# Kernel optimization log

Hardware: AMD Instinct MI355X
Metric: run time of the kernel (lower is better)

The kernel has to match this reference:

```python
import jax, jax.numpy as jnp
import numpy as np

B, N, D = 4, 512, 256  # batch, num_diseases, feature_dim == hidden_dim
H = 256                # hidden_dim
EPS = 1e-5

def _layernorm(x, g, b):
    m = jnp.mean(x, axis=-1, keepdims=True)
    v = jnp.mean((x - m) ** 2, axis=-1, keepdims=True)
    return (x - m) * jax.lax.rsqrt(v + EPS) * g + b

def setup_inputs() -> dict:
    key = jax.random.key(0)
    ks = jax.random.split(key, 16)
    s = 0.02
    return {
        "x": jax.random.normal(ks[0], (B, N, D), jnp.float32),
        "area_matrix": jax.random.uniform(ks[1], (B, N), jnp.float32),
        "co_occurrence": jax.random.uniform(ks[2], (N, N), jnp.float32),
        "Wq": jax.random.normal(ks[3], (H, D), jnp.float32) * s,
        "bq": jnp.zeros((H,), jnp.float32),
        "Wk": jax.random.normal(ks[4], (H, D), jnp.float32) * s,
        "bk": jnp.zeros((H,), jnp.float32),
        "Wv": jax.random.normal(ks[5], (H, D), jnp.float32) * s,
        "bv": jnp.zeros((H,), jnp.float32),
        "We1": jax.random.normal(ks[6], (H, 2), jnp.float32) * 0.5,
        "be1": jnp.zeros((H,), jnp.float32),
        "We2": jax.random.normal(ks[7], (1, H), jnp.float32) * s,
        "be2": jnp.zeros((1,), jnp.float32),
        "Wo": jax.random.normal(ks[8], (H, H), jnp.float32) * s,
        "bo": jnp.zeros((H,), jnp.float32),
        "g_ot": jnp.ones((H,), jnp.float32),
        "b_ot": jnp.zeros((H,), jnp.float32),
        "g1": jnp.ones((H,), jnp.float32),
        "b1": jnp.zeros((H,), jnp.float32),
        "g2": jnp.ones((H,), jnp.float32),
        "b2": jnp.zeros((H,), jnp.float32),
    }

def reference(x, area_matrix, co_occurrence, Wq, bq, Wk, bk, Wv, bv,
              We1, be1, We2, be2, Wo, bo, g_ot, b_ot, g1, b1, g2, b2):
    # projections: (B, N, H)
    q = jnp.einsum('bnd,hd->bnh', x, Wq) + bq
    k = jnp.einsum('bnd,hd->bnh', x, Wk) + bk
    v = jnp.einsum('bnd,hd->bnh', x, Wv) + bv
    attn_scores = jnp.einsum('bih,bjh->bij', q, k) / jnp.sqrt(jnp.float32(H))
    # edge inputs: (B, N, N, 2) = stack(broadcast area along last N, broadcast co-occ along batch)
    area = jnp.broadcast_to(area_matrix[:, :, None], (B, N, N))
    co = jnp.broadcast_to(co_occurrence[None], (B, N, N))
    edge_inputs = jnp.stack([area, co], axis=-1)
    h = jax.nn.relu(jnp.einsum('bije,he->bijh', edge_inputs, We1) + be1)
    edge_weights = jax.nn.sigmoid(jnp.einsum('bijh,oh->bijo', h, We2) + be2)[..., 0]
    attn_probs = jax.nn.softmax(attn_scores * edge_weights, axis=-1)  # dropout = identity (eval)
    out = jnp.einsum('bij,bjh->bih', attn_probs, v)
    out = _layernorm(out, g1, b1)
    out = jax.nn.relu(_layernorm(jnp.einsum('bnh,oh->bno', out, Wo) + bo, g_ot, b_ot))
    out = _layernorm(out + x, g2, b2)
    return out
```

## Files before the change

kernel.cpp:

```cpp
#include <hip/hip_runtime.h>

typedef unsigned short u16;
typedef unsigned int u32;

#define NB 4
#define NN 512
#define ND 256
#define NH 256
#define TI 4

typedef __attribute__((ext_vector_type(8))) short short8;
typedef __attribute__((ext_vector_type(4))) float f32x4;

__device__ __forceinline__ u16 bfq(float f) {
    u32 t; __builtin_memcpy(&t, &f, 4);
    u32 r = (t + 0x7FFFu + ((t >> 16) & 1u)) >> 16;
    return (u16)r;
}

__device__ __forceinline__ float waveReduceSum(float v) {
#pragma unroll
    for (int o = 32; o > 0; o >>= 1) v += __shfl_down(v, o);
    return v;
}

__device__ __forceinline__ void blockReduce8(float4& va, float4& vb, float4* red) {
#pragma unroll
    for (int o = 32; o > 0; o >>= 1) {
        va.x += __shfl_down(va.x, o); va.y += __shfl_down(va.y, o);
        va.z += __shfl_down(va.z, o); va.w += __shfl_down(va.w, o);
        vb.x += __shfl_down(vb.x, o); vb.y += __shfl_down(vb.y, o);
        vb.z += __shfl_down(vb.z, o); vb.w += __shfl_down(vb.w, o);
    }
    int wid = threadIdx.x >> 6;
    __syncthreads();
    if ((threadIdx.x & 63) == 0) { red[2 * wid] = va; red[2 * wid + 1] = vb; }
    __syncthreads();
    float4 ra = red[0], rb = red[1];
#pragma unroll
    for (int w = 1; w < 8; ++w) {
        float4 ua = red[2 * w], ub = red[2 * w + 1];
        ra.x += ua.x; ra.y += ua.y; ra.z += ua.z; ra.w += ua.w;
        rb.x += ub.x; rb.y += ub.y; rb.z += ub.z; rb.w += ub.w;
    }
    va = ra; vb = rb;
}

__global__ __launch_bounds__(256) void prep_kernel(
    const float* __restrict__ x, const float* __restrict__ Wq,
    const float* __restrict__ Wk, const float* __restrict__ Wv,
    const float* __restrict__ Wo,
    u16* __restrict__ xb, u16* __restrict__ wb)
{
    const int idx4 = (blockIdx.x * 256 + threadIdx.x) * 4;
    const float* src;
    u16* dst;
    int off;
    if (idx4 < 524288) { src = x; dst = xb; off = idx4; }
    else {
        int u = idx4 - 524288;
        int which = u >> 16; off = u & 65535;
        src = (which == 0) ? Wq : (which == 1) ? Wk : (which == 2) ? Wv : Wo;
        dst = wb + which * 65536;
    }
    float4 f = *(const float4*)(src + off);
    u32 lo = (u32)bfq(f.x) | ((u32)bfq(f.y) << 16);
    u32 hi = (u32)bfq(f.z) | ((u32)bfq(f.w) << 16);
    *(uint2*)(dst + off) = make_uint2(lo, hi);
}

__global__ __launch_bounds__(256) void qkv_mfma(
    const u16* __restrict__ xb, const u16* __restrict__ wb,
    const float* __restrict__ bq, const float* __restrict__ bk, const float* __restrict__ bv,
    u16* __restrict__ qb, u16* __restrict__ kb, u16* __restrict__ vt)
{
    const int lane = threadIdx.x & 63, wave = threadIdx.x >> 6;
    const int r0 = blockIdx.x * 64 + wave * 16;
    const int out0 = blockIdx.y * 16;
    const int which = blockIdx.y >> 4;
    const float* bia = (which == 0) ? bq : (which == 1) ? bk : bv;

    const int m = lane & 15, koff = (lane >> 4) * 8;
    const u16* Ap = xb + (size_t)(r0 + m) * 256 + koff;
    const u16* Bp = wb + which * 65536 + (size_t)((out0 & 255) + m) * 256 + koff;

    f32x4 acc = {0.f, 0.f, 0.f, 0.f};
#pragma unroll
    for (int ks = 0; ks < 8; ++ks) {
        short8 a  = *(const short8*)(Ap + ks * 32);
        short8 bb = *(const short8*)(Bp + ks * 32);
        acc = __builtin_amdgcn_mfma_f32_16x16x32_bf16(a, bb, acc, 0, 0, 0);
    }

    const int oc = (out0 + m) & 255;
    const float bias = bia[oc];
    const int rbase = r0 + (lane >> 4) * 4;
#pragma unroll
    for (int reg = 0; reg < 4; ++reg) {
        int R = rbase + reg;
        u16 val = bfq(acc[reg] + bias);
        if (which == 0)      qb[(size_t)R * 256 + oc] = val;
        else if (which == 1) kb[(size_t)R * 256 + oc] = val;
        else                 vt[((size_t)(R >> 9) * 256 + oc) * 512 + (R & 511)] = val;
    }
}

#define PSTR 520
#define YSTR 264
__global__ __launch_bounds__(512) void fused_kernel(
    const float* __restrict__ x, const float* __restrict__ area, const float* __restrict__ co,
    const float* __restrict__ We1, const float* __restrict__ be1,
    const float* __restrict__ We2, const float* __restrict__ be2,
    const u16* __restrict__ wob, const float* __restrict__ bo,
    const float* __restrict__ g_ot, const float* __restrict__ b_ot,
    const float* __restrict__ g1, const float* __restrict__ b1,
    const float* __restrict__ g2, const float* __restrict__ b2,
    const u16* __restrict__ qb, const u16* __restrict__ kb,
    const u16* __restrict__ vt, float* __restrict__ out)
{
    const int tid = threadIdx.x;
    const int b = blockIdx.x >> 7;
    const int i0 = (blockIdx.x & 127) << 2;
    const int lane = tid & 63, w = tid >> 6;

    __shared__ float histS[1024], histB[1024];
    __shared__ float pvbuf[1024];
    __shared__ u16 srow16[16 * PSTR];
    __shared__ u16 y16[16 * YSTR];
    __shared__ float4 red8b[16];
    __shared__ float sBaseS[4], sBaseB[4], redA[8], redB[8];

    const float be2f = be2[0];

    histS[tid] = 0.f; histS[tid + 512] = 0.f;
    histB[tid] = 0.f; histB[tid + 512] = 0.f;
    {
        u32* s32 = (u32*)srow16;
        for (int i = tid; i < 4160; i += 512) s32[i] = 0u;
        u32* y32 = (u32*)y16;
        for (int i = tid; i < 2112; i += 512) y32[i] = 0u;
    }
    __syncthreads();

    {
        const int s = tid >> 7, h0 = tid & 127;
        const float a = area[b * NN + i0 + s];
        float baS = 0.f, baB = 0.f;
#pragma unroll
        for (int k = 0; k < 2; ++k) {
            const int h = h0 + 128 * k;
            const float w10 = We1[2 * h], w11 = We1[2 * h + 1];
            const float w2v = We2[h], be1v = be1[h];
            const float al = fmaf(a, w10, be1v);
            const float sl = w11 * w2v, bb = al * w2v;
            if (w11 == 0.f) {
                if (al > 0.f) baB += bb;
            } else {
                float tt = -al / w11;
                if (w11 > 0.f) {
                    if (tt <= 0.f)      { baS += sl; baB += bb; }
                    else if (tt < 1.f) {
                        int u = (int)(tt * 256.f); u = u > 255 ? 255 : u;
                        atomicAdd(&histS[s * 256 + u], sl);
                        atomicAdd(&histB[s * 256 + u], bb);
                    }
                } else {
                    if (tt >= 1.f)      { baS += sl; baB += bb; }
                    else if (tt > 0.f) {
                        baS += sl; baB += bb;
                        int u = (int)(tt * 256.f); u = u > 255 ? 255 : u;
                        atomicAdd(&histS[s * 256 + u], -sl);
                        atomicAdd(&histB[s * 256 + u], -bb);
                    }
                }
            }
        }
        float rS = waveReduceSum(baS), rB = waveReduceSum(baB);
        if (lane == 0) { redA[w] = rS; redB[w] = rB; }
    }

    f32x4 sacc[4];
    {
        const int m = lane & 15, koff = (lane >> 4) * 8;
        const u16* Ap = qb + (size_t)(b * 512 + i0 + m) * 256 + koff;
        short8 afr[8];
#pragma unroll
        for (int ks = 0; ks < 8; ++ks) afr[ks] = *(const short8*)(Ap + ks * 32);
#pragma unroll
        for (int t = 0; t < 4; ++t) {
            const int j0 = (w * 4 + t) * 16;
            const u16* Bp = kb + (size_t)(b * 512 + j0 + m) * 256 + koff;
            f32x4 acc = {0.f, 0.f, 0.f, 0.f};
#pragma unroll
            for (int ks = 0; ks < 8; ++ks) {
                short8 bb = *(const short8*)(Bp + ks * 32);
                acc = __builtin_amdgcn_mfma_f32_16x16x32_bf16(afr[ks], bb, acc, 0, 0, 0);
            }
            sacc[t] = acc;
        }
    }
    __syncthreads();
    if (tid < 4) {
        sBaseS[tid] = redA[2 * tid] + redA[2 * tid + 1];
        sBaseB[tid] = redB[2 * tid] + redB[2 * tid + 1];
    }

    {
        const int s = w & 3;
        float* hp = (w < 4) ? histS : histB;
        float b0 = hp[s * 256 + 4 * lane + 0];
        float b1 = hp[s * 256 + 4 * lane + 1];
        float b2 = hp[s * 256 + 4 * lane + 2];
        float b3 = hp[s * 256 + 4 * lane + 3];
        float p0 = b0, p1 = p0 + b1, p2 = p1 + b2, p3 = p2 + b3;
        float incl = p3;
#pragma unroll
        for (int off = 1; off < 64; off <<= 1) {
            float t = __shfl_up(incl, off);
            if (lane >= off) incl += t;
        }
        float excl = incl - p3;
        hp[s * 256 + 4 * lane + 0] = p0 + excl;
        hp[s * 256 + 4 * lane + 1] = p1 + excl;
        hp[s * 256 + 4 * lane + 2] = p2 + excl;
        hp[s * 256 + 4 * lane + 3] = p3 + excl;
    }
    __syncthreads();

    if (lane < 16) {
#pragma unroll
        for (int t = 0; t < 4; ++t) {
            const int j = (w * 4 + t) * 16 + lane;
#pragma unroll
            for (int reg = 0; reg < 4; ++reg) {
                float c = co[(size_t)(i0 + reg) * NN + j];
                int u = (int)(c * 256.f); u = u > 255 ? 255 : u;
                float Sg = sBaseS[reg] + histS[reg * 256 + u];
                float Bg = sBaseB[reg] + histB[reg * 256 + u];
                float e = fmaf(c, Sg, Bg) + be2f;
                float ew = 1.f / (1.f + __expf(-e));
                srow16[reg * PSTR + j] = bfq(__expf(sacc[t][reg] * 0.0625f * ew));
            }
        }
    }
    __syncthreads();

    {
        const int m = lane & 15, koff = (lane >> 4) * 8;
        const int t0 = 2 * w, t1 = 2 * w + 1;
        const u16* B0p = vt + ((size_t)(b * 256 + t0 * 16 + m)) * 512 + koff;
        const u16* B1p = vt + ((size_t)(b * 256 + t1 * 16 + m)) * 512 + koff;
        const u16* Arow = srow16 + m * PSTR + koff;
        f32x4 acc0 = {0.f, 0.f, 0.f, 0.f}, acc1 = {0.f, 0.f, 0.f, 0.f};
#pragma unroll
        for (int ks = 0; ks < 16; ++ks) {
            short8 a  = *(const short8*)(Arow + ks * 32);
            short8 b0 = *(const short8*)(B0p + ks * 32);
            short8 b1 = *(const short8*)(B1p + ks * 32);
            acc0 = __builtin_amdgcn_mfma_f32_16x16x32_bf16(a, b0, acc0, 0, 0, 0);
            acc1 = __builtin_amdgcn_mfma_f32_16x16x32_bf16(a, b1, acc1, 0, 0, 0);
        }
        __syncthreads();
        if (lane < 16) {
#pragma unroll
            for (int reg = 0; reg < 4; ++reg) {
                pvbuf[reg * 256 + t0 * 16 + lane] = acc0[reg];
                pvbuf[reg * 256 + t1 * 16 + lane] = acc1[reg];
            }
        }
        __syncthreads();
    }

    const int hP = tid & 255, half = tid >> 8;
    float4 sa, sb;
    float accv[TI];
#pragma unroll
    for (int ti = 0; ti < TI; ++ti) {
        accv[ti] = (half == 0) ? pvbuf[ti * 256 + hP] : 0.f;
        ((float*)&sa)[ti] = accv[ti];
        ((float*)&sb)[ti] = accv[ti] * accv[ti];
    }
    blockReduce8(sa, sb, red8b);
    if (half == 0) {
        const float g1v = g1[hP], b1v = b1[hP];
#pragma unroll
        for (int ti = 0; ti < TI; ++ti) {
            float mean = ((const float*)&sa)[ti] * (1.f / 256.f);
            float var = fmaxf(((const float*)&sb)[ti] * (1.f / 256.f) - mean * mean, 0.f);
            y16[ti * YSTR + hP] = bfq((accv[ti] - mean) * rsqrtf(var + 1e-5f) * g1v + b1v);
        }
    }
    __syncthreads();

    {
        const int m = lane & 15, koff = (lane >> 4) * 8;
        const int t0 = 2 * w, t1 = 2 * w + 1;
        const u16* B0p = wob + (size_t)(t0 * 16 + m) * 256 + koff;
        const u16* B1p = wob + (size_t)(t1 * 16 + m) * 256 + koff;
        const u16* Arow = y16 + m * YSTR + koff;
        f32x4 acc0 = {0.f, 0.f, 0.f, 0.f}, acc1 = {0.f, 0.f, 0.f, 0.f};
#pragma unroll
        for (int ks = 0; ks < 8; ++ks) {
            short8 a  = *(const short8*)(Arow + ks * 32);
            short8 b0 = *(const short8*)(B0p + ks * 32);
            short8 b1 = *(const short8*)(B1p + ks * 32);
            acc0 = __builtin_amdgcn_mfma_f32_16x16x32_bf16(a, b0, acc0, 0, 0, 0);
            acc1 = __builtin_amdgcn_mfma_f32_16x16x32_bf16(a, b1, acc1, 0, 0, 0);
        }
        __syncthreads();
        if (lane < 16) {
#pragma unroll
            for (int reg = 0; reg < 4; ++reg) {
                pvbuf[reg * 256 + t0 * 16 + lane] = acc0[reg];
                pvbuf[reg * 256 + t1 * 16 + lane] = acc1[reg];
            }
        }
        __syncthreads();
    }

    float acc2[TI];
    {
        const float bov = (half == 0) ? bo[hP] : 0.f;
#pragma unroll
        for (int ti = 0; ti < TI; ++ti) {
            acc2[ti] = (half == 0) ? pvbuf[ti * 256 + hP] + bov : 0.f;
            ((float*)&sa)[ti] = acc2[ti];
            ((float*)&sb)[ti] = acc2[ti] * acc2[ti];
        }
    }
    blockReduce8(sa, sb, red8b);
    float z[TI];
    const float gotv = (half == 0) ? g_ot[hP] : 0.f;
    const float botv = (half == 0) ? b_ot[hP] : 0.f;
#pragma unroll
    for (int ti = 0; ti < TI; ++ti) {
        float mean = ((const float*)&sa)[ti] * (1.f / 256.f);
        float var = fmaxf(((const float*)&sb)[ti] * (1.f / 256.f) - mean * mean, 0.f);
        z[ti] = fmaxf((acc2[ti] - mean) * rsqrtf(var + 1e-5f) * gotv + botv, 0.f);
    }

    float tt[TI];
#pragma unroll
    for (int ti = 0; ti < TI; ++ti) {
        tt[ti] = (half == 0) ? z[ti] + x[(size_t)(b * NN + i0 + ti) * ND + hP] : 0.f;
        ((float*)&sa)[ti] = tt[ti]; ((float*)&sb)[ti] = tt[ti] * tt[ti];
    }
    blockReduce8(sa, sb, red8b);
    if (half == 0) {
        const float g2v = g2[hP], b2v = b2[hP];
#pragma unroll
        for (int ti = 0; ti < TI; ++ti) {
            float mean = ((const float*)&sa)[ti] * (1.f / 256.f);
            float var = fmaxf(((const float*)&sb)[ti] * (1.f / 256.f) - mean * mean, 0.f);
            float o = (tt[ti] - mean) * rsqrtf(var + 1e-5f) * g2v + b2v;
            out[(size_t)(b * NN + i0 + ti) * NH + hP] = o;
        }
    }
}

extern "C" void kernel_launch(void* const* d_in, const int* in_sizes, int n_in,
                              void* d_out, int out_size, void* d_ws, size_t ws_size,
                              hipStream_t stream) {
    const float* x    = (const float*)d_in[0];
    const float* area = (const float*)d_in[1];
    const float* co   = (const float*)d_in[2];
    const float* Wq   = (const float*)d_in[3];
    const float* bq   = (const float*)d_in[4];
    const float* Wk   = (const float*)d_in[5];
    const float* bk   = (const float*)d_in[6];
    const float* Wv   = (const float*)d_in[7];
    const float* bv   = (const float*)d_in[8];
    const float* We1  = (const float*)d_in[9];
    const float* be1  = (const float*)d_in[10];
    const float* We2  = (const float*)d_in[11];
    const float* be2  = (const float*)d_in[12];
    const float* Wo   = (const float*)d_in[13];
    const float* bo   = (const float*)d_in[14];
    const float* g_ot = (const float*)d_in[15];
    const float* b_ot = (const float*)d_in[16];
    const float* g1   = (const float*)d_in[17];
    const float* b1   = (const float*)d_in[18];
    const float* g2   = (const float*)d_in[19];
    const float* b2   = (const float*)d_in[20];

    u16*  xb  = (u16*)d_ws;
    u16*  wb  = xb + (size_t)2048 * 256;
    u16*  qb  = wb + (size_t)4 * 65536;
    u16*  kb  = qb + (size_t)2048 * 256;
    u16*  vt  = kb + (size_t)2048 * 256;

    prep_kernel<<<768, 256, 0, stream>>>(x, Wq, Wk, Wv, Wo, xb, wb);
    qkv_mfma<<<dim3(32, 48), 256, 0, stream>>>(xb, wb, bq, bk, bv, qb, kb, vt);
    fused_kernel<<<NB * NN / TI, 512, 0, stream>>>(x, area, co, We1, be1, We2, be2,
                                                   wb + 3 * 65536, bo,
                                                   g_ot, b_ot, g1, b1, g2, b2,
                                                   qb, kb, vt, (float*)d_out);
}
```

Measured before the change: 162.0 us.

## Prefetch global loads early, double-buffer K fragments, spread edge-weight work across lanes

Loads of the Q and K fragments, the co-occurrence values, x, and all per-channel parameters are moved to the top of the kernel so their latency overlaps the histogram phase. The QK^T loop now double-buffers K fragments in two halves so loads overlap the MFMAs. The edge-weight and exp step uses all 64 lanes via shuffles instead of only 16. Two barriers before the pvbuf writes are removed, and launch bounds now request 4 blocks. Register pressure rises from holding the prefetched values, and the occupancy hint may cause spills.

```diff
diff --git a/kernel.cpp b/kernel.cpp
--- a/kernel.cpp
+++ b/kernel.cpp
@@ -107,7 +107,7 @@
 
 #define PSTR 520
 #define YSTR 264
-__global__ __launch_bounds__(512) void fused_kernel(
+__global__ __launch_bounds__(512, 4) void fused_kernel(
     const float* __restrict__ x, const float* __restrict__ area, const float* __restrict__ co,
     const float* __restrict__ We1, const float* __restrict__ be1,
     const float* __restrict__ We2, const float* __restrict__ be2,
@@ -122,6 +122,8 @@
     const int b = blockIdx.x >> 7;
     const int i0 = (blockIdx.x & 127) << 2;
     const int lane = tid & 63, w = tid >> 6;
+    const int g = lane >> 4, c = lane & 15;
+    const int hP = tid & 255, half = tid >> 8;
 
     __shared__ float histS[1024], histB[1024];
     __shared__ float pvbuf[1024];
@@ -130,6 +132,32 @@
     __shared__ float4 red8b[16];
     __shared__ float sBaseS[4], sBaseB[4], redA[8], redB[8];
 
+    const int m = lane & 15, koff = (lane >> 4) * 8;
+    const u16* Ap    = qb + (size_t)(b * 512 + i0 + m) * 256 + koff;
+    const u16* Kbase = kb + (size_t)(b * 512 + m) * 256 + koff;
+
+    short8 afr[8];
+#pragma unroll
+    for (int ks = 0; ks < 8; ++ks) afr[ks] = *(const short8*)(Ap + ks * 32);
+    short8 k0[4], k1[4];
+#pragma unroll
+    for (int ks = 0; ks < 4; ++ks)
+        k0[ks] = *(const short8*)(Kbase + (size_t)(w * 4) * 16 * 256 + ks * 32);
+
+    float cov[4];
+#pragma unroll
+    for (int t = 0; t < 4; ++t)
+        cov[t] = co[(size_t)(i0 + g) * NN + (w * 4 + t) * 16 + c];
+
+    float xv[TI];
+#pragma unroll
+    for (int ti = 0; ti < TI; ++ti)
+        xv[ti] = x[(size_t)(b * NN + i0 + ti) * ND + hP];
+
+    const float bov  = bo[hP];
+    const float g1v  = g1[hP],  b1v  = b1[hP];
+    const float gotv = g_ot[hP], botv = b_ot[hP];
+    const float g2v  = g2[hP],  b2v  = b2[hP];
     const float be2f = be2[0];
 
     histS[tid] = 0.f; histS[tid + 512] = 0.f;
@@ -181,21 +209,23 @@
 
     f32x4 sacc[4];
     {
-        const int m = lane & 15, koff = (lane >> 4) * 8;
-        const u16* Ap = qb + (size_t)(b * 512 + i0 + m) * 256 + koff;
-        short8 afr[8];
-#pragma unroll
-        for (int ks = 0; ks < 8; ++ks) afr[ks] = *(const short8*)(Ap + ks * 32);
 #pragma unroll
         for (int t = 0; t < 4; ++t) {
-            const int j0 = (w * 4 + t) * 16;
-            const u16* Bp = kb + (size_t)(b * 512 + j0 + m) * 256 + koff;
+            const u16* Bp = Kbase + (size_t)(w * 4 + t) * 16 * 256;
+#pragma unroll
+            for (int ks = 0; ks < 4; ++ks) k1[ks] = *(const short8*)(Bp + (ks + 4) * 32);
             f32x4 acc = {0.f, 0.f, 0.f, 0.f};
 #pragma unroll
-            for (int ks = 0; ks < 8; ++ks) {
-                short8 bb = *(const short8*)(Bp + ks * 32);
-                acc = __builtin_amdgcn_mfma_f32_16x16x32_bf16(afr[ks], bb, acc, 0, 0, 0);
+            for (int ks = 0; ks < 4; ++ks)
+                acc = __builtin_amdgcn_mfma_f32_16x16x32_bf16(afr[ks], k0[ks], acc, 0, 0, 0);
+            if (t < 3) {
+                const u16* Bn = Kbase + (size_t)(w * 4 + t + 1) * 16 * 256;
+#pragma unroll
+                for (int ks = 0; ks < 4; ++ks) k0[ks] = *(const short8*)(Bn + ks * 32);
             }
+#pragma unroll
+            for (int ks = 0; ks < 4; ++ks)
+                acc = __builtin_amdgcn_mfma_f32_16x16x32_bf16(afr[ks + 4], k1[ks], acc, 0, 0, 0);
             sacc[t] = acc;
         }
     }
@@ -227,26 +257,27 @@
     }
     __syncthreads();
 
-    if (lane < 16) {
+    {
 #pragma unroll
         for (int t = 0; t < 4; ++t) {
-            const int j = (w * 4 + t) * 16 + lane;
-#pragma unroll
-            for (int reg = 0; reg < 4; ++reg) {
-                float c = co[(size_t)(i0 + reg) * NN + j];
-                int u = (int)(c * 256.f); u = u > 255 ? 255 : u;
-                float Sg = sBaseS[reg] + histS[reg * 256 + u];
-                float Bg = sBaseB[reg] + histB[reg * 256 + u];
-                float e = fmaf(c, Sg, Bg) + be2f;
-                float ew = 1.f / (1.f + __expf(-e));
-                srow16[reg * PSTR + j] = bfq(__expf(sacc[t][reg] * 0.0625f * ew));
-            }
-        }
-    }
-    __syncthreads();
-
-    {
-        const int m = lane & 15, koff = (lane >> 4) * 8;
+            const int j = (w * 4 + t) * 16 + c;
+            float s0 = __shfl(sacc[t][0], c);
+            float s1 = __shfl(sacc[t][1], c);
+            float s2 = __shfl(sacc[t][2], c);
+            float s3 = __shfl(sacc[t][3], c);
+            float sv = (g == 0) ? s0 : (g == 1) ? s1 : (g == 2) ? s2 : s3;
+            float cc = cov[t];
+            int u = (int)(cc * 256.f); u = u > 255 ? 255 : u;
+            float Sg = sBaseS[g] + histS[g * 256 + u];
+            float Bg = sBaseB[g] + histB[g * 256 + u];
+            float e = fmaf(cc, Sg, Bg) + be2f;
+            float ew = 1.f / (1.f + __expf(-e));
+            srow16[g * PSTR + j] = bfq(__expf(sv * 0.0625f * ew));
+        }
+    }
+    __syncthreads();
+
+    {
         const int t0 = 2 * w, t1 = 2 * w + 1;
         const u16* B0p = vt + ((size_t)(b * 256 + t0 * 16 + m)) * 512 + koff;
         const u16* B1p = vt + ((size_t)(b * 256 + t1 * 16 + m)) * 512 + koff;
@@ -260,7 +291,6 @@
             acc0 = __builtin_amdgcn_mfma_f32_16x16x32_bf16(a, b0, acc0, 0, 0, 0);
             acc1 = __builtin_amdgcn_mfma_f32_16x16x32_bf16(a, b1, acc1, 0, 0, 0);
         }
-        __syncthreads();
         if (lane < 16) {
 #pragma unroll
             for (int reg = 0; reg < 4; ++reg) {
@@ -271,7 +301,6 @@
         __syncthreads();
     }
 
-    const int hP = tid & 255, half = tid >> 8;
     float4 sa, sb;
     float accv[TI];
 #pragma unroll
@@ -282,7 +311,6 @@
     }
     blockReduce8(sa, sb, red8b);
     if (half == 0) {
-        const float g1v = g1[hP], b1v = b1[hP];
 #pragma unroll
         for (int ti = 0; ti < TI; ++ti) {
             float mean = ((const float*)&sa)[ti] * (1.f / 256.f);
@@ -293,7 +321,6 @@
     __syncthreads();
 
     {
-        const int m = lane & 15, koff = (lane >> 4) * 8;
         const int t0 = 2 * w, t1 = 2 * w + 1;
         const u16* B0p = wob + (size_t)(t0 * 16 + m) * 256 + koff;
         const u16* B1p = wob + (size_t)(t1 * 16 + m) * 256 + koff;
@@ -307,7 +334,6 @@
             acc0 = __builtin_amdgcn_mfma_f32_16x16x32_bf16(a, b0, acc0, 0, 0, 0);
             acc1 = __builtin_amdgcn_mfma_f32_16x16x32_bf16(a, b1, acc1, 0, 0, 0);
         }
-        __syncthreads();
         if (lane < 16) {
 #pragma unroll
             for (int reg = 0; reg < 4; ++reg) {
@@ -319,19 +345,14 @@
     }
 
     float acc2[TI];
-    {
-        const float bov = (half == 0) ? bo[hP] : 0.f;
-#pragma unroll
-        for (int ti = 0; ti < TI; ++ti) {
-            acc2[ti] = (half == 0) ? pvbuf[ti * 256 + hP] + bov : 0.f;
-            ((float*)&sa)[ti] = acc2[ti];
-            ((float*)&sb)[ti] = acc2[ti] * acc2[ti];
-        }
+#pragma unroll
+    for (int ti = 0; ti < TI; ++ti) {
+        acc2[ti] = (half == 0) ? pvbuf[ti * 256 + hP] + bov : 0.f;
+        ((float*)&sa)[ti] = acc2[ti];
+        ((float*)&sb)[ti] = acc2[ti] * acc2[ti];
     }
     blockReduce8(sa, sb, red8b);
     float z[TI];
-    const float gotv = (half == 0) ? g_ot[hP] : 0.f;
-    const float botv = (half == 0) ? b_ot[hP] : 0.f;
 #pragma unroll
     for (int ti = 0; ti < TI; ++ti) {
         float mean = ((const float*)&sa)[ti] * (1.f / 256.f);
@@ -342,12 +363,11 @@
     float tt[TI];
 #pragma unroll
     for (int ti = 0; ti < TI; ++ti) {
-        tt[ti] = (half == 0) ? z[ti] + x[(size_t)(b * NN + i0 + ti) * ND + hP] : 0.f;
+        tt[ti] = (half == 0) ? z[ti] + xv[ti] : 0.f;
         ((float*)&sa)[ti] = tt[ti]; ((float*)&sb)[ti] = tt[ti] * tt[ti];
     }
     blockReduce8(sa, sb, red8b);
     if (half == 0) {
-        const float g2v = g2[hP], b2v = b2[hP];
 #pragma unroll
         for (int ti = 0; ti < TI; ++ti) {
             float mean = ((const float*)&sa)[ti] * (1.f / 256.f);
```

Result: no change. 161.3 us (-0.4%).
